# Kernel optimization log

Measured on AMD Instinct MI355X. Metric: run time of the kernel, lower is better.

Reference implementation:

```python
import jax, jax.numpy as jnp
import numpy as np

HEADS = 8
DIM_HEAD = 64
SCALE = DIM_HEAD ** (-0.5)


def setup_inputs() -> dict:
    key = jax.random.key(0)
    k1, k2, k3, k4 = jax.random.split(key, 4)
    B, H, W, n, dim = 2, 64, 64, 8, 512
    inner = HEADS * DIM_HEAD  # 512
    x = jax.random.normal(k1, (B, H, W, n, dim), dtype=jnp.float32)
    mask = jax.random.uniform(k2, (B, H, W, 1, n, n), dtype=jnp.float32)
    w_qkv = jax.random.normal(k3, (dim, 3 * inner), dtype=jnp.float32) * 0.02
    w_out = jax.random.normal(k4, (inner, dim), dtype=jnp.float32) * 0.02
    b_out = jnp.zeros((dim,), dtype=jnp.float32)
    return {"x": x, "mask": mask, "w_qkv": w_qkv, "w_out": w_out, "b_out": b_out}


def reference(x, mask, w_qkv, w_out, b_out):
    B, H, W, n, dim = x.shape
    inner = HEADS * DIM_HEAD
    qkv = x @ w_qkv  # [B,H,W,n,3*inner]
    q, k, v = jnp.split(qkv, 3, axis=-1)

    def to_heads(t):
        # 'B H W n (h d) -> B H W h n d'
        t = t.reshape(B, H, W, n, HEADS, DIM_HEAD)
        return jnp.swapaxes(t, 3, 4)

    q, k, v = to_heads(q), to_heads(k), to_heads(v)
    dots = jnp.einsum('bxyhnd,bxyhmd->bxyhnm', q, k) * SCALE
    dots = dots * mask  # multiplicative mask pre-softmax
    attn = jax.nn.softmax(dots, axis=-1)
    out = jnp.einsum('bxyhnm,bxyhmd->bxyhnd', attn, v)
    # 'B H W h n d -> B H W n (h d)'
    out = jnp.swapaxes(out, 3, 4).reshape(B, H, W, n, inner)
    return out @ w_out + b_out
```

## Files before the change

### kernel.cpp

```cpp
#include <hip/hip_runtime.h>
#include <hip/hip_bf16.h>

#define NROWS 65536
#define DIM   512
#define SCALE_ 0.125f

typedef short bf16x8 __attribute__((ext_vector_type(8)));
typedef unsigned short u16x8 __attribute__((ext_vector_type(8)));
typedef float f32x4 __attribute__((ext_vector_type(4)));

__device__ __forceinline__ unsigned short f2bf(float f) {
  union { float f; unsigned u; } v; v.f = f;
  unsigned r = v.u + 0x7FFFu + ((v.u >> 16) & 1u);
  return (unsigned short)(r >> 16);
}
__device__ __forceinline__ float bf2f(unsigned short b) {
  union { unsigned u; float f; } v; v.u = ((unsigned)b) << 16;
  return v.f;
}

__global__ void prep_kernel(const float* __restrict__ wqkv,
                            const float* __restrict__ wout,
                            unsigned short* __restrict__ wqkvT,
                            unsigned short* __restrict__ woutT) {
  int idx = blockIdx.x * 256 + threadIdx.x;
  if (idx < 1536 * 512) {
    int j = idx >> 9, c = idx & 511;
    wqkvT[idx] = f2bf(wqkv[(size_t)c * 1536 + j]);
  } else {
    int k2 = idx - 1536 * 512;
    int n = k2 >> 9, c = k2 & 511;
    woutT[k2] = f2bf(wout[(size_t)c * 512 + n]);
  }
}

__global__ __launch_bounds__(256, 2)
void qkv_attn_kernel(const float* __restrict__ x,
                     const float* __restrict__ mask,
                     const unsigned short* __restrict__ wqkvT,
                     unsigned short* __restrict__ attn_out) {
  __shared__ __align__(16) unsigned char smem[57344];
  unsigned short* A_lds = (unsigned short*)smem;
  unsigned short* B_lds = (unsigned short*)(smem + 18432);
  unsigned short* C_lds = (unsigned short*)smem;
  float*          D_lds = (float*)(smem + 53248);

  const int t = threadIdx.x;
  const int lane = t & 63;
  const int wave = t >> 6;
  const int wm = wave >> 1, wn = wave & 1;
  const int fr = lane & 15, fq = lane >> 4;

  const int per = gridDim.x >> 3;
  const int lin = (blockIdx.x & 7) * per + (blockIdx.x >> 3);
  const int mtile = lin >> 3;
  const int head  = lin & 7;
  const int r0 = mtile * 128;

  f32x4 acc[4][6];
  const f32x4 z4 = {0.f, 0.f, 0.f, 0.f};
  #pragma unroll
  for (int m = 0; m < 4; ++m)
    #pragma unroll
    for (int n = 0; n < 6; ++n) acc[m][n] = z4;

  for (int kt = 0; kt < 8; ++kt) {
    const int k0 = kt * 64;
    #pragma unroll
    for (int i2 = 0; i2 < 8; ++i2) {
      int c = t + (i2 << 8);
      int row = c >> 4, q = c & 15;
      float4 v = *(const float4*)(x + (size_t)(r0 + row) * DIM + k0 + q * 4);
      ushort4 p;
      p.x = f2bf(v.x); p.y = f2bf(v.y); p.z = f2bf(v.z); p.w = f2bf(v.w);
      *(ushort4*)(A_lds + row * 72 + q * 4) = p;
    }
    #pragma unroll
    for (int i2 = 0; i2 < 6; ++i2) {
      int c = t + (i2 << 8);
      int n = c >> 3, wi = c & 7;
      int g = n >> 6, j = n & 63;
      int jg = g * 512 + head * 64 + j;
      *(uint4*)(B_lds + n * 72 + wi * 8) =
          *(const uint4*)(wqkvT + (size_t)jg * 512 + k0 + wi * 8);
    }
    __syncthreads();
    #pragma unroll
    for (int kk = 0; kk < 2; ++kk) {
      const int krd = kk * 32 + fq * 8;
      bf16x8 a[4], b[6];
      #pragma unroll
      for (int m = 0; m < 4; ++m)
        a[m] = *(const bf16x8*)(A_lds + (wm * 64 + m * 16 + fr) * 72 + krd);
      #pragma unroll
      for (int n = 0; n < 6; ++n)
        b[n] = *(const bf16x8*)(B_lds + (wn * 96 + n * 16 + fr) * 72 + krd);
      #pragma unroll
      for (int m = 0; m < 4; ++m)
        #pragma unroll
        for (int n = 0; n < 6; ++n)
          acc[m][n] = __builtin_amdgcn_mfma_f32_16x16x32_bf16(a[m], b[n], acc[m][n], 0, 0, 0);
    }
    __syncthreads();
  }

  #pragma unroll
  for (int m = 0; m < 4; ++m) {
    #pragma unroll
    for (int n = 0; n < 6; ++n) {
      int col = wn * 96 + n * 16 + fr;
      #pragma unroll
      for (int j = 0; j < 4; ++j) {
        int row = wm * 64 + m * 16 + fq * 4 + j;
        C_lds[row * 208 + col] = f2bf(acc[m][n][j]);
      }
    }
  }
  __syncthreads();

  const int px = t >> 4, tp = t & 15;
  const int qi = tp >> 1;
  const int half = tp & 1;
  const int j0 = half * 4;
  const int rbase = px * 8;
  const int P = mtile * 16 + px;

  float dt[4];
  {
    const unsigned short* Qrow = C_lds + (rbase + qi) * 208;
    #pragma unroll
    for (int jj = 0; jj < 4; ++jj) {
      const unsigned short* Krow = C_lds + (rbase + j0 + jj) * 208 + 64;
      float s = 0.f;
      #pragma unroll
      for (int c8 = 0; c8 < 8; ++c8) {
        bf16x8 qv = *(const bf16x8*)(Qrow + c8 * 8);
        bf16x8 kv = *(const bf16x8*)(Krow + c8 * 8);
        #pragma unroll
        for (int e = 0; e < 8; ++e)
          s += bf2f((unsigned short)qv[e]) * bf2f((unsigned short)kv[e]);
      }
      dt[jj] = s;
    }
  }
  const float* mrow = mask + (size_t)P * 64 + qi * 8 + j0;
  #pragma unroll
  for (int jj = 0; jj < 4; ++jj)
    D_lds[px * 64 + qi * 8 + j0 + jj] = dt[jj] * SCALE_ * mrow[jj];
  __syncthreads();

  if (tp < 8) {
    float* dr = D_lds + px * 64 + tp * 8;
    float mx = dr[0];
    #pragma unroll
    for (int j = 1; j < 8; ++j) mx = fmaxf(mx, dr[j]);
    float e[8], sum = 0.f;
    #pragma unroll
    for (int j = 0; j < 8; ++j) { e[j] = __expf(dr[j] - mx); sum += e[j]; }
    float inv = 1.f / sum;
    #pragma unroll
    for (int j = 0; j < 8; ++j) dr[j] = e[j] * inv;
  }
  __syncthreads();

  float av[8];
  #pragma unroll
  for (int j = 0; j < 8; ++j) av[j] = D_lds[px * 64 + qi * 8 + j];
  float ov[32];
  #pragma unroll
  for (int d = 0; d < 32; ++d) ov[d] = 0.f;
  #pragma unroll
  for (int j = 0; j < 8; ++j) {
    const unsigned short* Vrow = C_lds + (rbase + j) * 208 + 128 + half * 32;
    #pragma unroll
    for (int c8 = 0; c8 < 4; ++c8) {
      bf16x8 vv = *(const bf16x8*)(Vrow + c8 * 8);
      #pragma unroll
      for (int e = 0; e < 8; ++e)
        ov[c8 * 8 + e] += av[j] * bf2f((unsigned short)vv[e]);
    }
  }
  unsigned short* orow = attn_out + (size_t)(r0 + rbase + qi) * 512 + head * 64 + half * 32;
  #pragma unroll
  for (int c8 = 0; c8 < 4; ++c8) {
    u16x8 p;
    #pragma unroll
    for (int e = 0; e < 8; ++e) p[e] = f2bf(ov[c8 * 8 + e]);
    *(u16x8*)(orow + c8 * 8) = p;
  }
}

__global__ __launch_bounds__(256, 2)
void outproj_kernel(const unsigned short* __restrict__ attn,
                    const unsigned short* __restrict__ woutT,
                    const float* __restrict__ bias,
                    float* __restrict__ out) {
  __shared__ __align__(16) unsigned short A2[128 * 72];
  __shared__ __align__(16) unsigned short B2[128 * 72];
  const int t = threadIdx.x;
  const int lane = t & 63, wave = t >> 6;
  const int wm = wave >> 1, wn = wave & 1;
  const int fr = lane & 15, fq = lane >> 4;

  const int per = gridDim.x >> 3;
  const int lin = (blockIdx.x & 7) * per + (blockIdx.x >> 3);
  const int mtile = lin >> 2, nt = lin & 3;
  const int r0 = mtile * 128, n0 = nt * 128;

  f32x4 acc[4][4];
  const f32x4 z4 = {0.f, 0.f, 0.f, 0.f};
  #pragma unroll
  for (int m = 0; m < 4; ++m)
    #pragma unroll
    for (int n = 0; n < 4; ++n) acc[m][n] = z4;

  for (int kt = 0; kt < 8; ++kt) {
    const int k0 = kt * 64;
    #pragma unroll
    for (int i2 = 0; i2 < 4; ++i2) {
      int c = t + (i2 << 8);
      int row = c >> 3, wi = c & 7;
      *(uint4*)(A2 + row * 72 + wi * 8) =
          *(const uint4*)(attn + (size_t)(r0 + row) * 512 + k0 + wi * 8);
      *(uint4*)(B2 + row * 72 + wi * 8) =
          *(const uint4*)(woutT + (size_t)(n0 + row) * 512 + k0 + wi * 8);
    }
    __syncthreads();
    #pragma unroll
    for (int kk = 0; kk < 2; ++kk) {
      const int krd = kk * 32 + fq * 8;
      bf16x8 a[4], b[4];
      #pragma unroll
      for (int m = 0; m < 4; ++m)
        a[m] = *(const bf16x8*)(A2 + (wm * 64 + m * 16 + fr) * 72 + krd);
      #pragma unroll
      for (int n = 0; n < 4; ++n)
        b[n] = *(const bf16x8*)(B2 + (wn * 64 + n * 16 + fr) * 72 + krd);
      #pragma unroll
      for (int m = 0; m < 4; ++m)
        #pragma unroll
        for (int n = 0; n < 4; ++n)
          acc[m][n] = __builtin_amdgcn_mfma_f32_16x16x32_bf16(a[m], b[n], acc[m][n], 0, 0, 0);
    }
    __syncthreads();
  }
  #pragma unroll
  for (int n = 0; n < 4; ++n) {
    int col = n0 + wn * 64 + n * 16 + fr;
    float bv = bias[col];
    #pragma unroll
    for (int m = 0; m < 4; ++m) {
      #pragma unroll
      for (int j = 0; j < 4; ++j) {
        int row = r0 + wm * 64 + m * 16 + fq * 4 + j;
        out[(size_t)row * 512 + col] = acc[m][n][j] + bv;
      }
    }
  }
}

extern "C" void kernel_launch(void* const* d_in, const int* in_sizes, int n_in,
                              void* d_out, int out_size, void* d_ws, size_t ws_size,
                              hipStream_t stream) {
  const float* x    = (const float*)d_in[0];
  const float* mask = (const float*)d_in[1];
  const float* wqkv = (const float*)d_in[2];
  const float* wout = (const float*)d_in[3];
  const float* bias = (const float*)d_in[4];
  float* out = (float*)d_out;

  unsigned char* ws = (unsigned char*)d_ws;
  unsigned short* attn  = (unsigned short*)ws;
  unsigned short* wqkvT = (unsigned short*)(ws + 67108864);
  unsigned short* woutT = (unsigned short*)(ws + 67108864 + 1572864);

  prep_kernel<<<4096, 256, 0, stream>>>(wqkv, wout, wqkvT, woutT);
  qkv_attn_kernel<<<4096, 256, 0, stream>>>(x, mask, wqkvT, attn);
  outproj_kernel<<<2048, 256, 0, stream>>>(attn, woutT, bias, out);
}
```

Measured before the change: 252.1 us.

## Double-buffer QKV GEMM with direct-to-LDS loads, pre-cast x, MFMA attention

Adds a separate pass that converts x to bf16 ahead of time. The QKV GEMM then streams bf16 x and weights straight into LDS with global_load_lds, using XOR-swizzled tiles and a double buffer so the next k-tile loads while the current one computes. The per-pixel attention is rewritten to use MFMA for QK^T and PV, with shuffle-based softmax and a transposed V tile. The cost is an extra 64MB read plus 64MB write pass over x, which may offset the GEMM gains. LDS use rises to 80KB, which may cap occupancy below the two blocks requested.

```diff
diff --git a/kernel.cpp b/kernel.cpp
--- a/kernel.cpp
+++ b/kernel.cpp
@@ -14,15 +14,15 @@
   unsigned r = v.u + 0x7FFFu + ((v.u >> 16) & 1u);
   return (unsigned short)(r >> 16);
 }
-__device__ __forceinline__ float bf2f(unsigned short b) {
-  union { unsigned u; float f; } v; v.u = ((unsigned)b) << 16;
-  return v.f;
-}
-
-__global__ void prep_kernel(const float* __restrict__ wqkv,
-                            const float* __restrict__ wout,
-                            unsigned short* __restrict__ wqkvT,
-                            unsigned short* __restrict__ woutT) {
+
+#define GLL16(gptr, lptr) \
+  __builtin_amdgcn_global_load_lds((const __attribute__((address_space(1))) void*)(gptr), \
+                                   (__attribute__((address_space(3))) void*)(lptr), 16, 0, 0)
+
+__global__ void prep_w_kernel(const float* __restrict__ wqkv,
+                              const float* __restrict__ wout,
+                              unsigned short* __restrict__ wqkvT,
+                              unsigned short* __restrict__ woutT) {
   int idx = blockIdx.x * 256 + threadIdx.x;
   if (idx < 1536 * 512) {
     int j = idx >> 9, c = idx & 511;
@@ -34,27 +34,36 @@
   }
 }
 
+__global__ void prep_x_kernel(const float* __restrict__ x,
+                              unsigned short* __restrict__ xb) {
+  size_t i = ((size_t)blockIdx.x * 256 + threadIdx.x) * 8;
+  float4 a = *(const float4*)(x + i);
+  float4 b = *(const float4*)(x + i + 4);
+  u16x8 p;
+  p[0] = f2bf(a.x); p[1] = f2bf(a.y); p[2] = f2bf(a.z); p[3] = f2bf(a.w);
+  p[4] = f2bf(b.x); p[5] = f2bf(b.y); p[6] = f2bf(b.z); p[7] = f2bf(b.w);
+  *(u16x8*)(xb + i) = p;
+}
+
+template<int AMODE>
 __global__ __launch_bounds__(256, 2)
 void qkv_attn_kernel(const float* __restrict__ x,
+                     const unsigned short* __restrict__ xb,
                      const float* __restrict__ mask,
                      const unsigned short* __restrict__ wqkvT,
                      unsigned short* __restrict__ attn_out) {
-  __shared__ __align__(16) unsigned char smem[57344];
-  unsigned short* A_lds = (unsigned short*)smem;
-  unsigned short* B_lds = (unsigned short*)(smem + 18432);
-  unsigned short* C_lds = (unsigned short*)smem;
-  float*          D_lds = (float*)(smem + 53248);
+  __shared__ __align__(16) unsigned char smem[81920];
 
   const int t = threadIdx.x;
-  const int lane = t & 63;
-  const int wave = t >> 6;
+  const int lane = t & 63, wave = t >> 6;
   const int wm = wave >> 1, wn = wave & 1;
   const int fr = lane & 15, fq = lane >> 4;
+  const int l8 = lane >> 3;
+  const int cswz = ((lane & 7) ^ l8) * 8;
 
   const int per = gridDim.x >> 3;
   const int lin = (blockIdx.x & 7) * per + (blockIdx.x >> 3);
-  const int mtile = lin >> 3;
-  const int head  = lin & 7;
+  const int mtile = lin >> 3, head = lin & 7;
   const int r0 = mtile * 128;
 
   f32x4 acc[4][6];
@@ -64,129 +73,162 @@
     #pragma unroll
     for (int n = 0; n < 6; ++n) acc[m][n] = z4;
 
+  auto STAGE = [&](int buf, int kt2) {
+    unsigned char* base = smem + buf * 40960;
+    const int k0 = kt2 * 64;
+    if constexpr (AMODE == 0) {
+      const unsigned short* gA = xb + (size_t)(r0 + l8) * 512 + k0 + cswz;
+      #pragma unroll
+      for (int i = 0; i < 4; ++i) {
+        int c = wave * 4 + i;
+        GLL16(gA + (size_t)c * 8 * 512, base + c * 1024);
+      }
+    } else {
+      #pragma unroll
+      for (int i2 = 0; i2 < 8; ++i2) {
+        int c = t + (i2 << 8);
+        int row = c >> 4, q = c & 15;
+        float4 v = *(const float4*)(x + (size_t)(r0 + row) * 512 + k0 + q * 4);
+        ushort4 p;
+        p.x = f2bf(v.x); p.y = f2bf(v.y); p.z = f2bf(v.z); p.w = f2bf(v.w);
+        unsigned byte = (unsigned)row * 128 +
+                        ((((unsigned)(q >> 1)) << 4) ^ (((unsigned)(row & 7)) << 4)) +
+                        (unsigned)(q & 1) * 8;
+        *(ushort4*)(base + byte) = p;
+      }
+    }
+    const unsigned short* gB = wqkvT + k0 + cswz;
+    #pragma unroll
+    for (int i = 0; i < 6; ++i) {
+      int c = wave * 6 + i;
+      int n = c * 8 + l8;
+      int jg = ((n >> 6) << 9) + head * 64 + (n & 63);
+      GLL16(gB + (size_t)jg * 512, base + 16384 + c * 1024);
+    }
+  };
+
+  STAGE(0, 0);
+  asm volatile("s_waitcnt vmcnt(0)" ::: "memory");
+  __syncthreads();
+  int cur = 0;
+
   for (int kt = 0; kt < 8; ++kt) {
-    const int k0 = kt * 64;
-    #pragma unroll
-    for (int i2 = 0; i2 < 8; ++i2) {
-      int c = t + (i2 << 8);
-      int row = c >> 4, q = c & 15;
-      float4 v = *(const float4*)(x + (size_t)(r0 + row) * DIM + k0 + q * 4);
-      ushort4 p;
-      p.x = f2bf(v.x); p.y = f2bf(v.y); p.z = f2bf(v.z); p.w = f2bf(v.w);
-      *(ushort4*)(A_lds + row * 72 + q * 4) = p;
-    }
-    #pragma unroll
-    for (int i2 = 0; i2 < 6; ++i2) {
-      int c = t + (i2 << 8);
-      int n = c >> 3, wi = c & 7;
-      int g = n >> 6, j = n & 63;
-      int jg = g * 512 + head * 64 + j;
-      *(uint4*)(B_lds + n * 72 + wi * 8) =
-          *(const uint4*)(wqkvT + (size_t)jg * 512 + k0 + wi * 8);
-    }
-    __syncthreads();
+    if (kt < 7) STAGE(cur ^ 1, kt + 1);
+    unsigned char* Ab = smem + cur * 40960;
+    unsigned char* Bb = Ab + 16384;
+    const unsigned xr = ((unsigned)(fr & 7)) << 4;
     #pragma unroll
     for (int kk = 0; kk < 2; ++kk) {
-      const int krd = kk * 32 + fq * 8;
+      const unsigned ko = ((unsigned)(kk * 64 + fq * 16)) ^ xr;
       bf16x8 a[4], b[6];
       #pragma unroll
       for (int m = 0; m < 4; ++m)
-        a[m] = *(const bf16x8*)(A_lds + (wm * 64 + m * 16 + fr) * 72 + krd);
+        a[m] = *(const bf16x8*)(Ab + (unsigned)(wm * 64 + m * 16 + fr) * 128 + ko);
       #pragma unroll
       for (int n = 0; n < 6; ++n)
-        b[n] = *(const bf16x8*)(B_lds + (wn * 96 + n * 16 + fr) * 72 + krd);
+        b[n] = *(const bf16x8*)(Bb + (unsigned)(wn * 96 + n * 16 + fr) * 128 + ko);
       #pragma unroll
       for (int m = 0; m < 4; ++m)
         #pragma unroll
         for (int n = 0; n < 6; ++n)
           acc[m][n] = __builtin_amdgcn_mfma_f32_16x16x32_bf16(a[m], b[n], acc[m][n], 0, 0, 0);
     }
+    asm volatile("s_waitcnt vmcnt(0)" ::: "memory");
     __syncthreads();
-  }
-
-  #pragma unroll
-  for (int m = 0; m < 4; ++m) {
-    #pragma unroll
-    for (int n = 0; n < 6; ++n) {
-      int col = wn * 96 + n * 16 + fr;
-      #pragma unroll
-      for (int j = 0; j < 4; ++j) {
-        int row = wm * 64 + m * 16 + fq * 4 + j;
-        C_lds[row * 208 + col] = f2bf(acc[m][n][j]);
+    cur ^= 1;
+  }
+
+  unsigned short* Qs = (unsigned short*)smem;
+  unsigned short* Ks = (unsigned short*)(smem + 16384);
+  unsigned short* VT = (unsigned short*)(smem + 32768);
+  unsigned short* Pl = (unsigned short*)(smem + 52224);
+
+  {
+    int d = t >> 2, q = t & 3;
+    ushort4 z; z.x = 0; z.y = 0; z.z = 0; z.w = 0;
+    *(ushort4*)(VT + d * 152 + 128 + q * 4) = z;
+  }
+  #pragma unroll
+  for (int n = 0; n < 6; ++n) {
+    int col = wn * 96 + n * 16 + fr;
+    #pragma unroll
+    for (int m = 0; m < 4; ++m) {
+      if (col < 128) {
+        unsigned short* T = (col < 64) ? Qs : Ks;
+        unsigned cc = (unsigned)(col & 63);
+        #pragma unroll
+        for (int r = 0; r < 4; ++r) {
+          int row = wm * 64 + m * 16 + fq * 4 + r;
+          unsigned byte = (unsigned)row * 128 + ((cc * 2) ^ (((unsigned)(row & 7)) << 4));
+          *(unsigned short*)((unsigned char*)T + byte) = f2bf(acc[m][n][r]);
+        }
+      } else {
+        int d = col - 128;
+        ushort4 p;
+        p.x = f2bf(acc[m][n][0]); p.y = f2bf(acc[m][n][1]);
+        p.z = f2bf(acc[m][n][2]); p.w = f2bf(acc[m][n][3]);
+        *(ushort4*)(VT + d * 152 + (wm * 64 + m * 16 + fq * 4)) = p;
       }
     }
   }
   __syncthreads();
 
-  const int px = t >> 4, tp = t & 15;
-  const int qi = tp >> 1;
-  const int half = tp & 1;
-  const int j0 = half * 4;
-  const int rbase = px * 8;
-  const int P = mtile * 16 + px;
-
-  float dt[4];
-  {
-    const unsigned short* Qrow = C_lds + (rbase + qi) * 208;
-    #pragma unroll
-    for (int jj = 0; jj < 4; ++jj) {
-      const unsigned short* Krow = C_lds + (rbase + j0 + jj) * 208 + 64;
-      float s = 0.f;
-      #pragma unroll
-      for (int c8 = 0; c8 < 8; ++c8) {
-        bf16x8 qv = *(const bf16x8*)(Qrow + c8 * 8);
-        bf16x8 kv = *(const bf16x8*)(Krow + c8 * 8);
-        #pragma unroll
-        for (int e = 0; e < 8; ++e)
-          s += bf2f((unsigned short)qv[e]) * bf2f((unsigned short)kv[e]);
-      }
-      dt[jj] = s;
-    }
-  }
-  const float* mrow = mask + (size_t)P * 64 + qi * 8 + j0;
-  #pragma unroll
-  for (int jj = 0; jj < 4; ++jj)
-    D_lds[px * 64 + qi * 8 + j0 + jj] = dt[jj] * SCALE_ * mrow[jj];
-  __syncthreads();
-
-  if (tp < 8) {
-    float* dr = D_lds + px * 64 + tp * 8;
-    float mx = dr[0];
-    #pragma unroll
-    for (int j = 1; j < 8; ++j) mx = fmaxf(mx, dr[j]);
-    float e[8], sum = 0.f;
-    #pragma unroll
-    for (int j = 0; j < 8; ++j) { e[j] = __expf(dr[j] - mx); sum += e[j]; }
-    float inv = 1.f / sum;
-    #pragma unroll
-    for (int j = 0; j < 8; ++j) dr[j] = e[j] * inv;
-  }
-  __syncthreads();
-
-  float av[8];
-  #pragma unroll
-  for (int j = 0; j < 8; ++j) av[j] = D_lds[px * 64 + qi * 8 + j];
-  float ov[32];
-  #pragma unroll
-  for (int d = 0; d < 32; ++d) ov[d] = 0.f;
-  #pragma unroll
-  for (int j = 0; j < 8; ++j) {
-    const unsigned short* Vrow = C_lds + (rbase + j) * 208 + 128 + half * 32;
-    #pragma unroll
-    for (int c8 = 0; c8 < 4; ++c8) {
-      bf16x8 vv = *(const bf16x8*)(Vrow + c8 * 8);
-      #pragma unroll
-      for (int e = 0; e < 8; ++e)
-        ov[c8 * 8 + e] += av[j] * bf2f((unsigned short)vv[e]);
-    }
-  }
-  unsigned short* orow = attn_out + (size_t)(r0 + rbase + qi) * 512 + head * 64 + half * 32;
-  #pragma unroll
-  for (int c8 = 0; c8 < 4; ++c8) {
-    u16x8 p;
-    #pragma unroll
-    for (int e = 0; e < 8; ++e) p[e] = f2bf(ov[c8 * 8 + e]);
-    *(u16x8*)(orow + c8 * 8) = p;
+  #pragma unroll
+  for (int pp = 0; pp < 2; ++pp) {
+    const int pair = wave * 2 + pp;
+    const unsigned rbyte = (unsigned)(pair * 16 + fr) * 128;
+    const unsigned xrp = ((unsigned)(fr & 7)) << 4;
+    f32x4 s = {0.f, 0.f, 0.f, 0.f};
+    #pragma unroll
+    for (int kk = 0; kk < 2; ++kk) {
+      const unsigned ko = ((unsigned)(kk * 64 + fq * 16)) ^ xrp;
+      bf16x8 qf = *(const bf16x8*)((unsigned char*)Qs + rbyte + ko);
+      bf16x8 kf = *(const bf16x8*)((unsigned char*)Ks + rbyte + ko);
+      s = __builtin_amdgcn_mfma_f32_16x16x32_bf16(qf, kf, s, 0, 0, 0);
+    }
+    float p4[4];
+    #pragma unroll
+    for (int r = 0; r < 4; ++r) {
+      int row = fq * 4 + r;
+      bool valid = (row >> 3) == (fr >> 3);
+      int Pg = mtile * 16 + pair * 2 + (row >> 3);
+      float mv = mask[(size_t)Pg * 64 + (row & 7) * 8 + (fr & 7)];
+      p4[r] = valid ? s[r] * SCALE_ * mv : -3.0e38f;
+    }
+    #pragma unroll
+    for (int r = 0; r < 4; ++r) {
+      float v = p4[r];
+      float mx = v;
+      mx = fmaxf(mx, __shfl_xor(mx, 1));
+      mx = fmaxf(mx, __shfl_xor(mx, 2));
+      mx = fmaxf(mx, __shfl_xor(mx, 4));
+      float e = __expf(v - mx);
+      float sm = e;
+      sm += __shfl_xor(sm, 1);
+      sm += __shfl_xor(sm, 2);
+      sm += __shfl_xor(sm, 4);
+      p4[r] = e / sm;
+    }
+    #pragma unroll
+    for (int r = 0; r < 4; ++r) {
+      int row = fq * 4 + r;
+      bool valid = (row >> 3) == (fr >> 3);
+      Pl[pair * 640 + row * 40 + fr] = valid ? f2bf(p4[r]) : (unsigned short)0;
+      Pl[pair * 640 + row * 40 + 16 + fr] = 0;
+    }
+    #pragma unroll
+    for (int dblk = 0; dblk < 4; ++dblk) {
+      bf16x8 af = *(const bf16x8*)((unsigned char*)VT +
+                    (unsigned)(dblk * 16 + fr) * 304 + (unsigned)(pair * 32 + fq * 16));
+      bf16x8 bf = *(const bf16x8*)((unsigned char*)Pl +
+                    (unsigned)pair * 1280 + (unsigned)fr * 80 + (unsigned)fq * 16);
+      f32x4 o = {0.f, 0.f, 0.f, 0.f};
+      o = __builtin_amdgcn_mfma_f32_16x16x32_bf16(af, bf, o, 0, 0, 0);
+      ushort4 pk;
+      pk.x = f2bf(o[0]); pk.y = f2bf(o[1]); pk.z = f2bf(o[2]); pk.w = f2bf(o[3]);
+      *(ushort4*)(attn_out + (size_t)(r0 + pair * 16 + fr) * 512 +
+                  head * 64 + dblk * 16 + fq * 4) = pk;
+    }
   }
 }
 
@@ -273,8 +315,15 @@
   unsigned short* attn  = (unsigned short*)ws;
   unsigned short* wqkvT = (unsigned short*)(ws + 67108864);
   unsigned short* woutT = (unsigned short*)(ws + 67108864 + 1572864);
-
-  prep_kernel<<<4096, 256, 0, stream>>>(wqkv, wout, wqkvT, woutT);
-  qkv_attn_kernel<<<4096, 256, 0, stream>>>(x, mask, wqkvT, attn);
+  unsigned short* xb    = (unsigned short*)(ws + 67108864 + 1572864 + 524288);
+  const size_t need_xb = 67108864ull + 1572864ull + 524288ull + 67108864ull;
+
+  prep_w_kernel<<<4096, 256, 0, stream>>>(wqkv, wout, wqkvT, woutT);
+  if (ws_size >= need_xb) {
+    prep_x_kernel<<<16384, 256, 0, stream>>>(x, xb);
+    qkv_attn_kernel<0><<<4096, 256, 0, stream>>>(x, xb, mask, wqkvT, attn);
+  } else {
+    qkv_attn_kernel<1><<<4096, 256, 0, stream>>>(x, xb, mask, wqkvT, attn);
+  }
   outproj_kernel<<<2048, 256, 0, stream>>>(attn, woutT, bias, out);
 }
```

Result: faster. 238.9 us (-5.2%).
